# Optimization experiments

Hardware: AMD Instinct MI355X
Metric: run time of the kernel (lower is better)

The kernel has to match this reference:

```python
import jax, jax.numpy as jnp
import numpy as np

B, S, HIDDEN, NH = 2, 2048, 1024, 16
D = HIDDEN // NH  # 64
PHYS_W, CONS_W = 0.2, 0.15
LN_EPS = 1e-5


def _layernorm(x, gamma, beta):
    mu = jnp.mean(x, axis=-1, keepdims=True)
    var = jnp.mean(jnp.square(x - mu), axis=-1, keepdims=True)
    return (x - mu) * jax.lax.rsqrt(var + LN_EPS) * gamma + beta


def setup_inputs() -> dict:
    key = jax.random.key(0)
    ks = jax.random.split(key, 12)
    s = 0.02
    return {
        "cnn_features": jax.random.normal(ks[0], (B, S, HIDDEN), jnp.float32),
        "llm_features": jax.random.normal(ks[1], (B, S, HIDDEN), jnp.float32),
        # Linear weights stored [in, out] so y = x @ W + b (torch's W.T)
        "Wq": jax.random.normal(ks[2], (HIDDEN, HIDDEN), jnp.float32) * s,
        "bq": jnp.zeros((HIDDEN,), jnp.float32),
        "Wk": jax.random.normal(ks[3], (HIDDEN, HIDDEN), jnp.float32) * s,
        "bk": jnp.zeros((HIDDEN,), jnp.float32),
        "Wv": jax.random.normal(ks[4], (HIDDEN, HIDDEN), jnp.float32) * s,
        "bv": jnp.zeros((HIDDEN,), jnp.float32),
        "Wo": jax.random.normal(ks[5], (HIDDEN, HIDDEN), jnp.float32) * s,
        "bo": jnp.zeros((HIDDEN,), jnp.float32),
        "energy_emb": jax.random.normal(ks[6], (1, 1, HIDDEN), jnp.float32),
        "mass_emb": jax.random.normal(ks[7], (1, 1, HIDDEN), jnp.float32),
        "momentum_emb": jax.random.normal(ks[8], (1, 1, HIDDEN), jnp.float32),
        "gamma": jnp.ones((HIDDEN,), jnp.float32),
        "beta": jnp.zeros((HIDDEN,), jnp.float32),
    }


def reference(cnn_features, llm_features, Wq, bq, Wk, bk, Wv, bv, Wo, bo,
              energy_emb, mass_emb, momentum_emb, gamma, beta):
    Bsz, Sc, _ = cnn_features.shape
    Sl = llm_features.shape[1]

    def attn(q_in, kv_in):
        Sq, Sk = q_in.shape[1], kv_in.shape[1]
        Q = (q_in @ Wq + bq).reshape(Bsz, Sq, NH, D).transpose(0, 2, 1, 3)   # bhqd
        K = (kv_in @ Wk + bk).reshape(Bsz, Sk, NH, D).transpose(0, 2, 1, 3)  # bhkd
        V = (kv_in @ Wv + bv).reshape(Bsz, Sk, NH, D).transpose(0, 2, 1, 3)  # bhkd
        scores = jnp.einsum('bhqd,bhkd->bhqk', Q, K) / np.float32(np.sqrt(D))
        # physics biases: require Sq == Sk (elementwise Q*K), shape [B,H,Sq,1]
        energy_bias = jnp.sum(Q * K, axis=-1, keepdims=True) * PHYS_W
        mass_bias = jnp.mean(Q + K, axis=-1, keepdims=True) * CONS_W
        attn_w = jax.nn.softmax(scores + energy_bias + mass_bias, axis=-1)
        attended = jnp.einsum('bhqk,bhkd->bhqd', attn_w, V)
        attended = attended.transpose(0, 2, 1, 3).reshape(Bsz, Sq, HIDDEN)
        out = attended @ Wo + bo
        return _layernorm(q_in + out, gamma, beta)

    phys = jnp.concatenate([
        jnp.broadcast_to(energy_emb, (Bsz, 1, HIDDEN)),
        jnp.broadcast_to(mass_emb, (Bsz, 1, HIDDEN)),
        jnp.broadcast_to(momentum_emb, (Bsz, 1, HIDDEN)),
    ], axis=1)  # [B, 3, HIDDEN]
    aug_cnn = jnp.concatenate([cnn_features, phys], axis=1)  # [B, Sc+3, H]
    aug_llm = jnp.concatenate([llm_features, phys], axis=1)  # [B, Sl+3, H]

    cnn_att = attn(aug_cnn, aug_llm)
    llm_att = attn(aug_llm, aug_cnn)
    return cnn_att[:, :Sc, :], llm_att[:, :Sl, :]
```

## Files before the change

### kernel.cpp

```cpp
#include <hip/hip_runtime.h>

#define BN 2
#define SS 2048
#define SA 2051
#define HID 1024
#define NHD 16
#define DH 64
#define VTLD 8320
#define KSTR 72
#define VSTR 40
#define MFMA16 __builtin_amdgcn_mfma_f32_16x16x32_bf16
#define QSCALE 0.18033688011112042f

typedef __attribute__((ext_vector_type(4))) float floatx4;
typedef __attribute__((ext_vector_type(8))) short bf16x8;
typedef __attribute__((ext_vector_type(2))) unsigned uintx2;

__device__ __forceinline__ float bf2f(short s) {
  union { unsigned u; float f; } v; v.u = ((unsigned)(unsigned short)s) << 16; return v.f;
}
__device__ __forceinline__ short f2bf(float f) {
  union { float f; unsigned u; } v; v.f = f;
  unsigned u = v.u;
  u += 0x7FFF + ((u >> 16) & 1);
  return (short)(u >> 16);
}
__device__ __forceinline__ unsigned pack2(float lo, float hi) {
  unsigned ul = __float_as_uint(lo) + 0x8000u;
  unsigned uh = __float_as_uint(hi) + 0x8000u;
  return __builtin_amdgcn_perm(uh, ul, 0x07060302u);
}
__device__ __forceinline__ unsigned cvtpk(float lo, float hi) {
  unsigned r;
  asm("v_cvt_pk_bf16_f32 %0, %1, %2" : "=v"(r) : "v"(lo), "v"(hi));
  return r;
}
__device__ __forceinline__ float exp2fast(float x) {
#if __has_builtin(__builtin_amdgcn_exp2f)
  return __builtin_amdgcn_exp2f(x);
#else
  float r; asm("v_exp_f32 %0, %1" : "=v"(r) : "v"(x)); return r;
#endif
}
__device__ __forceinline__ uintx2 qtrans(unsigned A, unsigned B) {
  auto t = __builtin_amdgcn_permlane32_swap(A, B, false, false);
  auto u = __builtin_amdgcn_permlane16_swap(t[0], t[1], false, false);
  uintx2 r; r[0] = u[0]; r[1] = u[1];
  return r;
}
__device__ __forceinline__ void gload16(const short* g, short* l) {
  __builtin_amdgcn_global_load_lds(
      (const __attribute__((address_space(1))) void*)g,
      (__attribute__((address_space(3))) void*)l, 16, 0, 0);
}
__device__ __forceinline__ bool in_is_f32(const unsigned* graw) {
  return graw[0] == 0x3F800000u;
}

__global__ __launch_bounds__(256) void convert_in(const void* __restrict__ src, long off,
                                                  short* __restrict__ dst, int n,
                                                  const unsigned* __restrict__ graw) {
  bool f32 = in_is_f32(graw);
  int i = (blockIdx.x * 256 + threadIdx.x) * 4;
  int stride = gridDim.x * 1024;
  if (f32) {
    const float* s = (const float*)src + off;
    for (; i < n; i += stride) {
      float4 v = *(const float4*)(s + i);
      short4 o; o.x = f2bf(v.x); o.y = f2bf(v.y); o.z = f2bf(v.z); o.w = f2bf(v.w);
      *(short4*)(dst + i) = o;
    }
  } else {
    const short* s = (const short*)src + off;
    for (; i < n; i += stride)
      *(short4*)(dst + i) = *(const short4*)(s + i);
  }
}

__global__ __launch_bounds__(256) void convert_small(
    const void* s0, const void* s1, const void* s2, const void* s3,
    const void* s4, const void* s5, const void* s6, const void* s7,
    const void* s8, short* __restrict__ dst, const unsigned* __restrict__ graw) {
  bool f32 = in_is_f32(graw);
  const void* srcs[9] = {s0, s1, s2, s3, s4, s5, s6, s7, s8};
  const void* s = srcs[blockIdx.x];
  short* d = dst + (size_t)blockIdx.x * 1024;
  for (int i = threadIdx.x; i < 1024; i += 256)
    d[i] = f32 ? f2bf(((const float*)s)[i]) : ((const short*)s)[i];
}

__global__ __launch_bounds__(256) void conv_wt(const void* __restrict__ W,
    short* __restrict__ WT, const unsigned* __restrict__ graw) {
  __shared__ short tile[32][33];
  bool f32 = in_is_f32(graw);
  int n0 = blockIdx.x * 32, k0 = blockIdx.y * 32;
  int tx = threadIdx.x & 31, ty = threadIdx.x >> 5;
#pragma unroll
  for (int i = 0; i < 4; i++) {
    int k = k0 + ty + i*8;
    short v = f32 ? f2bf(((const float*)W)[(size_t)k * HID + n0 + tx])
                  : ((const short*)W)[(size_t)k * HID + n0 + tx];
    tile[ty + i*8][tx] = v;
  }
  __syncthreads();
#pragma unroll
  for (int i = 0; i < 4; i++)
    WT[(size_t)(n0 + ty + i*8) * HID + k0 + tx] = tile[tx][ty + i*8];
}

__device__ __forceinline__ void gemm_core_2ph(
    const short* apr0, const short* apr1,
    const short* bpr0, const short* bpr1,
    short* sA, short* sB, int wave, int l16, int quad, int msub, int nsub,
    floatx4 acc[4][4]) {
  gload16(apr0, sA + wave*512);  gload16(apr1, sA + 2048 + wave*512);
  gload16(bpr0, sB + wave*512);  gload16(bpr1, sB + 2048 + wave*512);
  int cur = 0;
  for (int k0 = 0; k0 < HID; k0 += 32) {
    if (k0 + 32 < HID) {
      int nx = cur ^ 1;
      gload16(apr0 + k0 + 32, sA + nx*4096 + wave*512);
      gload16(apr1 + k0 + 32, sA + nx*4096 + 2048 + wave*512);
      gload16(bpr0 + k0 + 32, sB + nx*4096 + wave*512);
      gload16(bpr1 + k0 + 32, sB + nx*4096 + 2048 + wave*512);
      asm volatile("s_waitcnt vmcnt(4)" ::: "memory");
    } else {
      asm volatile("s_waitcnt vmcnt(0)" ::: "memory");
    }
    __builtin_amdgcn_s_barrier();
    __builtin_amdgcn_sched_barrier(0);
    const short* cA = sA + cur*4096;
    const short* cB = sB + cur*4096;
    bf16x8 af[4], bf_[4];
#pragma unroll
    for (int i = 0; i < 4; i++) {
      af[i]  = *(const bf16x8*)(cA + (msub + i*16 + l16)*32 + quad*8);
      bf_[i] = *(const bf16x8*)(cB + (nsub + i*16 + l16)*32 + quad*8);
    }
#pragma unroll
    for (int mi = 0; mi < 4; mi++)
#pragma unroll
      for (int ni = 0; ni < 4; ni++)
        acc[mi][ni] = MFMA16(af[mi], bf_[ni], acc[mi][ni], 0, 0, 0);
    __builtin_amdgcn_sched_barrier(0);
    __builtin_amdgcn_s_barrier();
    __builtin_amdgcn_sched_barrier(0);
    cur ^= 1;
  }
}

__global__ __launch_bounds__(256) void gemm_qkv(
    const short* __restrict__ Xa, const short* __restrict__ WqT,
    const short* __restrict__ WkT, const short* __restrict__ WvT,
    const short* __restrict__ embB, const short* __restrict__ bqB,
    const short* __restrict__ bkB, const short* __restrict__ bvB,
    short* __restrict__ Qa, short* __restrict__ Ka, short* __restrict__ VT) {
  __shared__ __align__(16) short sA[2*4096];
  __shared__ __align__(16) short sB[2*4096];
  int t = threadIdx.x;
  int wave = t >> 6, lane = t & 63, l16 = lane & 15, quad = lane >> 4;
  int bid = blockIdx.x;
  int swz = (bid & 7) * 194 + (bid >> 3);

  const short *A, *B, *bias; short* out; long ldc;
  int m0, n0, tailA, tailB, bias_row; float scale;
  if (swz < 512) {
    A = Xa; B = WqT; bias = bqB; out = Qa; ldc = HID;
    m0 = (swz >> 3) * 128; n0 = (swz & 7) * 128;
    tailA = 0; tailB = 0; bias_row = 0; scale = QSCALE;
  } else if (swz < 1032) {
    int id = swz - 512;
    A = Xa; B = WkT; bias = bkB; out = Ka; ldc = HID;
    m0 = (id >> 3) * 128; n0 = (id & 7) * 128;
    tailA = 1; tailB = 0; bias_row = 0; scale = 1.f;
  } else {
    int id = swz - 1032;
    A = WvT; B = Xa; bias = bvB; out = VT; ldc = VTLD;
    m0 = (id / 65) * 128; n0 = (id % 65) * 128;
    tailA = 0; tailB = 1; bias_row = 1; scale = 1.f;
  }
  int msub = (wave >> 1) * 64, nsub = (wave & 1) * 64;

  const short* apr[2]; const short* bpr[2];
#pragma unroll
  for (int rep = 0; rep < 2; rep++) {
    int cid = rep * 256 + t;
    int row = cid >> 2, kc = (cid & 3) * 8;
    int ra = m0 + row;
    const short* ap;
    if (tailA && ra >= 8192) ap = embB + (size_t)((ra > 8194 ? 8194 : ra) - 8192) * 1024;
    else                     ap = A + (size_t)ra * HID;
    int rb = n0 + row;
    const short* bp;
    if (tailB && rb >= 8192) bp = embB + (size_t)((rb > 8194 ? 8194 : rb) - 8192) * 1024;
    else                     bp = B + (size_t)rb * HID;
    apr[rep] = ap + kc; bpr[rep] = bp + kc;
  }

  floatx4 acc[4][4] = {};
  gemm_core_2ph(apr[0], apr[1], bpr[0], bpr[1], sA, sB,
                wave, l16, quad, msub, nsub, acc);

#pragma unroll
  for (int mi = 0; mi < 4; mi++)
#pragma unroll
    for (int ni = 0; ni < 4; ni++) {
      int col = n0 + nsub + ni*16 + l16;
      float bcol = bias_row ? 0.f : bf2f(bias[col]);
#pragma unroll
      for (int r = 0; r < 4; r++) {
        int m = m0 + msub + mi*16 + quad*4 + r;
        float v = (acc[mi][ni][r] + (bias_row ? bf2f(bias[m]) : bcol)) * scale;
        out[(size_t)m * ldc + col] = f2bf(v);
      }
    }
}

__global__ __launch_bounds__(256) void gemm_bf(
    const short* __restrict__ A, const short* __restrict__ B,
    const short* __restrict__ bias, float scale,
    float* __restrict__ out32,
    const void* __restrict__ rc0, const void* __restrict__ rc1,
    const unsigned* __restrict__ graw) {
  __shared__ __align__(16) short sA[2*4096];
  __shared__ __align__(16) short sB[2*4096];
  int t = threadIdx.x;
  int wave = t >> 6, lane = t & 63, l16 = lane & 15, quad = lane >> 4;
  int nwg = gridDim.x * gridDim.y;
  int bid = blockIdx.y * gridDim.x + blockIdx.x;
  int cpx = nwg >> 3;
  int swz = (bid & 7) * cpx + (bid >> 3);
  int bx = swz % gridDim.x, by = swz / gridDim.x;
  int m0 = by * 128, n0 = bx * 128;
  int msub = (wave >> 1) * 64, nsub = (wave & 1) * 64;

  const short* apr[2]; const short* bpr[2];
#pragma unroll
  for (int rep = 0; rep < 2; rep++) {
    int cid = rep * 256 + t;
    int row = cid >> 2, kc = (cid & 3) * 8;
    apr[rep] = A + (size_t)(m0 + row) * HID + kc;
    bpr[rep] = B + (size_t)(n0 + row) * HID + kc;
  }

  floatx4 acc[4][4] = {};
  gemm_core_2ph(apr[0], apr[1], bpr[0], bpr[1], sA, sB,
                wave, l16, quad, msub, nsub, acc);

  bool f32in = in_is_f32(graw);
#pragma unroll
  for (int mi = 0; mi < 4; mi++)
#pragma unroll
    for (int ni = 0; ni < 4; ni++) {
      int col = n0 + nsub + ni*16 + l16;
      float bcol = bf2f(bias[col]);
#pragma unroll
      for (int r = 0; r < 4; r++) {
        int m = m0 + msub + mi*16 + quad*4 + r;
        float v = (acc[mi][ni][r] + bcol) * scale;
        float res;
        if (f32in) res = ((const float*)(m < 4096 ? rc0 : rc1))[(size_t)(m & 4095) * HID + col];
        else       res = bf2f(((const short*)(m < 4096 ? rc0 : rc1))[(size_t)(m & 4095) * HID + col]);
        out32[(size_t)m * HID + col] = v + res;
      }
    }
}

__global__ __launch_bounds__(256, 4) void flash3(
    const short* __restrict__ Qa, const short* __restrict__ Ka,
    const short* __restrict__ VTa, short* __restrict__ att) {
  __shared__ __align__(16) short sK0[32*KSTR], sK1[32*KSTR];
  __shared__ __align__(16) short sV0[64*VSTR], sV1[64*VSTR];
  int t = threadIdx.x, wave = t >> 6, lane = t & 63;
  int l16 = lane & 15, quad = lane >> 4;
  int bid = blockIdx.x;
  int swz = (bid & 7) * 128 + (bid >> 3);
  int qt  = swz & 15;
  int h   = (swz >> 4) & 15;
  int sb  = swz >> 8;
  int side = sb >> 1, b = sb & 1;
  int qrow0 = side * 4096 + b * 2048;
  int kvb = (side ^ 1) * 4096 + b * 2048;
  int q0 = qt * 128 + wave * 32;

  const short* qp0 = Qa + (size_t)(qrow0 + q0 + l16) * HID + h*DH + quad*8;
  const short* qp1 = qp0 + 16 * HID;
  bf16x8 qa0 = *(const bf16x8*)qp0, qb0 = *(const bf16x8*)(qp0 + 32);
  bf16x8 qa1 = *(const bf16x8*)qp1, qb1 = *(const bf16x8*)(qp1 + 32);

  float rs0 = 0.f, rs1 = 0.f;
  floatx4 oA[4] = {}, oB[4] = {};

  int krow = t >> 3, kc8 = (t & 7) * 8;
  int vrow = t >> 2, vc8 = (t & 3) * 8;
  const short* kgp = Ka + (size_t)(kvb + krow) * HID + h*DH + kc8;
  const short* vgp = VTa + (size_t)(h*DH + vrow) * VTLD + kvb + vc8;
  bf16x8 kreg = *(const bf16x8*)kgp;
  bf16x8 vreg = *(const bf16x8*)vgp;
  short *kw = sK0, *vw = sV0, *ka = sK1, *va = sV1;

  for (int kv0 = 0; kv0 < 2048; kv0 += 32) {
    *(bf16x8*)(kw + krow*KSTR + kc8) = kreg;
    *(bf16x8*)(vw + vrow*VSTR + vc8) = vreg;
    __syncthreads();
    kgp += 32*HID; vgp += 32;
    kreg = *(const bf16x8*)kgp;
    vreg = *(const bf16x8*)vgp;

    bf16x8 k00 = *(const bf16x8*)(kw + l16*KSTR + quad*8);
    bf16x8 k01 = *(const bf16x8*)(kw + l16*KSTR + 32 + quad*8);
    bf16x8 k10 = *(const bf16x8*)(kw + (16 + l16)*KSTR + quad*8);
    bf16x8 k11 = *(const bf16x8*)(kw + (16 + l16)*KSTR + 32 + quad*8);
    bf16x8 v0 = *(const bf16x8*)(vw + l16*VSTR + quad*8);
    bf16x8 v1 = *(const bf16x8*)(vw + (16 + l16)*VSTR + quad*8);
    bf16x8 v2 = *(const bf16x8*)(vw + (32 + l16)*VSTR + quad*8);
    bf16x8 v3 = *(const bf16x8*)(vw + (48 + l16)*VSTR + quad*8);

    floatx4 s00 = {}, s10 = {}, s01 = {}, s11 = {};
    __builtin_amdgcn_s_setprio(1);
    s00 = MFMA16(k00, qa0, s00, 0, 0, 0); s00 = MFMA16(k01, qb0, s00, 0, 0, 0);
    s10 = MFMA16(k10, qa0, s10, 0, 0, 0); s10 = MFMA16(k11, qb0, s10, 0, 0, 0);
    s01 = MFMA16(k00, qa1, s01, 0, 0, 0); s01 = MFMA16(k01, qb1, s01, 0, 0, 0);
    s11 = MFMA16(k10, qa1, s11, 0, 0, 0); s11 = MFMA16(k11, qb1, s11, 0, 0, 0);
    __builtin_amdgcn_s_setprio(0);

    floatx4 p00, p10, p01, p11;
#pragma unroll
    for (int r = 0; r < 4; r++) {
      p00[r] = exp2fast(s00[r]); p10[r] = exp2fast(s10[r]);
      p01[r] = exp2fast(s01[r]); p11[r] = exp2fast(s11[r]);
    }
    rs0 += ((p00[0]+p00[1])+(p00[2]+p00[3])) + ((p10[0]+p10[1])+(p10[2]+p10[3]));
    rs1 += ((p01[0]+p01[1])+(p01[2]+p01[3])) + ((p11[0]+p11[1])+(p11[2]+p11[3]));

    unsigned pc00 = cvtpk(p00[0], p00[1]), pc01 = cvtpk(p00[2], p00[3]);
    unsigned pc10 = cvtpk(p10[0], p10[1]), pc11 = cvtpk(p10[2], p10[3]);
    unsigned pd00 = cvtpk(p01[0], p01[1]), pd01 = cvtpk(p01[2], p01[3]);
    unsigned pd10 = cvtpk(p11[0], p11[1]), pd11 = cvtpk(p11[2], p11[3]);
    uintx2 uA0 = qtrans(pc00, pc10);
    uintx2 uA1 = qtrans(pc01, pc11);
    uintx2 uB0 = qtrans(pd00, pd10);
    uintx2 uB1 = qtrans(pd01, pd11);
    union { unsigned u[4]; bf16x8 v; } pf0, pf1;
    pf0.u[0] = uA0[0]; pf0.u[1] = uA1[0]; pf0.u[2] = uA0[1]; pf0.u[3] = uA1[1];
    pf1.u[0] = uB0[0]; pf1.u[1] = uB1[0]; pf1.u[2] = uB0[1]; pf1.u[3] = uB1[1];

    __builtin_amdgcn_s_setprio(1);
    oA[0] = MFMA16(v0, pf0.v, oA[0], 0, 0, 0);
    oA[1] = MFMA16(v1, pf0.v, oA[1], 0, 0, 0);
    oA[2] = MFMA16(v2, pf0.v, oA[2], 0, 0, 0);
    oA[3] = MFMA16(v3, pf0.v, oA[3], 0, 0, 0);
    oB[0] = MFMA16(v0, pf1.v, oB[0], 0, 0, 0);
    oB[1] = MFMA16(v1, pf1.v, oB[1], 0, 0, 0);
    oB[2] = MFMA16(v2, pf1.v, oB[2], 0, 0, 0);
    oB[3] = MFMA16(v3, pf1.v, oB[3], 0, 0, 0);
    __builtin_amdgcn_s_setprio(0);

    short* tk = kw; kw = ka; ka = tk;
    short* tv = vw; vw = va; va = tv;
  }

  {
    int er = l16 < 2 ? l16 : 2;
    const short* kpt = Ka + (size_t)(8192 + er) * HID + h*DH + quad*8;
    bf16x8 tk0 = *(const bf16x8*)kpt;
    bf16x8 tk1 = *(const bf16x8*)(kpt + 32);
    floatx4 s00 = {}, s01 = {};
    s00 = MFMA16(tk0, qa0, s00, 0, 0, 0); s00 = MFMA16(tk1, qb0, s00, 0, 0, 0);
    s01 = MFMA16(tk0, qa1, s01, 0, 0, 0); s01 = MFMA16(tk1, qb1, s01, 0, 0, 0);
    floatx4 p00, p01;
#pragma unroll
    for (int r = 0; r < 4; r++) {
      bool val = (quad == 0) && (r < 3);
      p00[r] = val ? exp2fast(s00[r]) : 0.f;
      p01[r] = val ? exp2fast(s01[r]) : 0.f;
    }
    rs0 += (p00[0]+p00[1]) + (p00[2]+p00[3]);
    rs1 += (p01[0]+p01[1]) + (p01[2]+p01[3]);
    unsigned pc00 = cvtpk(p00[0], p00[1]), pc01 = cvtpk(p00[2], p00[3]);
    unsigned pd00 = cvtpk(p01[0], p01[1]), pd01 = cvtpk(p01[2], p01[3]);
    uintx2 uA0 = qtrans(pc00, 0u);
    uintx2 uA1 = qtrans(pc01, 0u);
    uintx2 uB0 = qtrans(pd00, 0u);
    uintx2 uB1 = qtrans(pd01, 0u);
    union { unsigned u[4]; bf16x8 v; } pf0, pf1;
    pf0.u[0] = uA0[0]; pf0.u[1] = uA1[0]; pf0.u[2] = uA0[1]; pf0.u[3] = uA1[1];
    pf1.u[0] = uB0[0]; pf1.u[1] = uB1[0]; pf1.u[2] = uB0[1]; pf1.u[3] = uB1[1];
    const short* vtp = VTa + (size_t)(h*DH + l16) * VTLD + 8192 + quad*8;
    bf16x8 v0 = *(const bf16x8*)vtp;
    bf16x8 v1 = *(const bf16x8*)(vtp + 16*VTLD);
    bf16x8 v2 = *(const bf16x8*)(vtp + 32*VTLD);
    bf16x8 v3 = *(const bf16x8*)(vtp + 48*VTLD);
    oA[0] = MFMA16(v0, pf0.v, oA[0], 0, 0, 0);
    oA[1] = MFMA16(v1, pf0.v, oA[1], 0, 0, 0);
    oA[2] = MFMA16(v2, pf0.v, oA[2], 0, 0, 0);
    oA[3] = MFMA16(v3, pf0.v, oA[3], 0, 0, 0);
    oB[0] = MFMA16(v0, pf1.v, oB[0], 0, 0, 0);
    oB[1] = MFMA16(v1, pf1.v, oB[1], 0, 0, 0);
    oB[2] = MFMA16(v2, pf1.v, oB[2], 0, 0, 0);
    oB[3] = MFMA16(v3, pf1.v, oB[3], 0, 0, 0);
  }

  rs0 += __shfl_xor(rs0, 16, 64); rs0 += __shfl_xor(rs0, 32, 64);
  rs1 += __shfl_xor(rs1, 16, 64); rs1 += __shfl_xor(rs1, 32, 64);
  float i0 = 1.f / rs0, i1 = 1.f / rs1;

  unsigned* ob0 = (unsigned*)(att + (size_t)(qrow0 + q0 + l16) * HID + h*DH + quad*4);
  unsigned* ob1 = (unsigned*)(att + (size_t)(qrow0 + q0 + 16 + l16) * HID + h*DH + quad*4);
#pragma unroll
  for (int n = 0; n < 4; n++) {
    ob0[n*8]     = pack2(oA[n][0]*i0, oA[n][1]*i0);
    ob0[n*8 + 1] = pack2(oA[n][2]*i0, oA[n][3]*i0);
    ob1[n*8]     = pack2(oB[n][0]*i1, oB[n][1]*i1);
    ob1[n*8 + 1] = pack2(oB[n][2]*i1, oB[n][3]*i1);
  }
}

__global__ __launch_bounds__(256) void ln_kernel(
    const float* __restrict__ y, const short* __restrict__ gamma,
    const short* __restrict__ beta, void* __restrict__ outp, long orow,
    const unsigned* __restrict__ graw) {
  bool f32o = in_is_f32(graw);
  int row = blockIdx.x;
  int t = threadIdx.x;
  const float* yr = y + (size_t)row * HID;
  float4 v = ((const float4*)yr)[t];
  float sum = v.x + v.y + v.z + v.w;
#pragma unroll
  for (int off = 32; off >= 1; off >>= 1) sum += __shfl_xor(sum, off, 64);
  __shared__ float red[8];
  int wave = t >> 6, lane = t & 63;
  if (lane == 0) red[wave] = sum;
  __syncthreads();
  float mu = (red[0] + red[1] + red[2] + red[3]) * (1.f/HID);
  float dx = v.x - mu, dy = v.y - mu, dz = v.z - mu, dw = v.w - mu;
  float sq = dx*dx + dy*dy + dz*dz + dw*dw;
#pragma unroll
  for (int off = 32; off >= 1; off >>= 1) sq += __shfl_xor(sq, off, 64);
  if (lane == 0) red[4 + wave] = sq;
  __syncthreads();
  float var = (red[4] + red[5] + red[6] + red[7]) * (1.f/HID);
  float inv = rsqrtf(var + 1e-5f);
  const short* g = gamma + t*4;
  const short* be = beta + t*4;
  float o0 = dx * inv * bf2f(g[0]) + bf2f(be[0]);
  float o1 = dy * inv * bf2f(g[1]) + bf2f(be[1]);
  float o2 = dz * inv * bf2f(g[2]) + bf2f(be[2]);
  float o3 = dw * inv * bf2f(g[3]) + bf2f(be[3]);
  size_t base = (size_t)(orow + row) * HID + t*4;
  if (f32o) {
    float4 ov = {o0, o1, o2, o3};
    *(float4*)((float*)outp + base) = ov;
  } else {
    short4 ov = {f2bf(o0), f2bf(o1), f2bf(o2), f2bf(o3)};
    *(short4*)((short*)outp + base) = ov;
  }
}

extern "C" void kernel_launch(void* const* d_in, const int* in_sizes, int n_in,
                              void* d_out, int out_size, void* d_ws, size_t ws_size,
                              hipStream_t stream) {
  const void* cnn = d_in[0];
  const void* llm = d_in[1];
  const void* Wq  = d_in[2];
  const void* bq  = d_in[3];
  const void* Wk  = d_in[4];
  const void* bk  = d_in[5];
  const void* Wv  = d_in[6];
  const void* bv  = d_in[7];
  const void* Wo  = d_in[8];
  const void* bo  = d_in[9];
  const void* ee  = d_in[10];
  const void* me  = d_in[11];
  const void* pe  = d_in[12];
  const void* gamma = d_in[13];
  const void* beta  = d_in[14];
  const unsigned* graw = (const unsigned*)gamma;
  (void)in_sizes; (void)n_in; (void)out_size; (void)ws_size;

  char* p = (char*)d_ws;
  auto alloc = [&](size_t bytes) { char* r = p; p += (bytes + 255) & ~(size_t)255; return r; };
  short* WqT = (short*)alloc((size_t)HID*HID*2);
  short* WkT = (short*)alloc((size_t)HID*HID*2);
  short* WvT = (short*)alloc((size_t)HID*HID*2);
  short* WoT = (short*)alloc((size_t)HID*HID*2);
  short* smallB = (short*)alloc(9 * 1024 * 2);
  short* Qa  = (short*)alloc((size_t)8192 * HID * 2);
  short* Ka  = (short*)alloc((size_t)8320 * HID * 2);
  short* VT  = (short*)alloc((size_t)HID * VTLD * 2);
  float* y   = (float*)Qa;
  short* att = (short*)d_out;
  short* Xa  = (short*)d_out + (size_t)8192 * HID;
  short* bqB = smallB;        short* bkB = smallB + 1024;
  short* bvB = smallB + 2048; short* boB = smallB + 3072;
  short* embB = smallB + 4096;
  short* gB  = smallB + 7168; short* bB  = smallB + 8192;

  dim3 tb(256);
  dim3 tg(32, 32);
  const int NF = 4096 * HID;

  convert_in<<<dim3(NF/1024), tb, 0, stream>>>(cnn, 0, Xa, NF, graw);
  convert_in<<<dim3(NF/1024), tb, 0, stream>>>(llm, 0, Xa + (size_t)NF, NF, graw);
  conv_wt<<<tg, tb, 0, stream>>>(Wq, WqT, graw);
  conv_wt<<<tg, tb, 0, stream>>>(Wk, WkT, graw);
  conv_wt<<<tg, tb, 0, stream>>>(Wv, WvT, graw);
  conv_wt<<<tg, tb, 0, stream>>>(Wo, WoT, graw);
  convert_small<<<dim3(9), tb, 0, stream>>>(bq, bk, bv, bo, ee, me, pe, gamma, beta,
                                            smallB, graw);

  gemm_qkv<<<dim3(1552), tb, 0, stream>>>(Xa, WqT, WkT, WvT, embB,
                                          bqB, bkB, bvB, Qa, Ka, VT);

  flash3<<<dim3(1024), tb, 0, stream>>>(Qa, Ka, VT, att);

  gemm_bf<<<dim3(8, 64), tb, 0, stream>>>(att, WoT, boB, 1.f, y, cnn, llm, graw);

  ln_kernel<<<dim3(8192), tb, 0, stream>>>(y, gB, bB, d_out, 0, graw);
}
```

Before: 371.4 us.

## Merge conversion launches and swizzle GEMM LDS tile layout to avoid bank conflicts

Result: faster. 353.6 us (-4.8%).

```diff
diff --git a/kernel.cpp b/kernel.cpp
--- a/kernel.cpp
+++ b/kernel.cpp
@@ -57,23 +57,20 @@
   return graw[0] == 0x3F800000u;
 }
 
-__global__ __launch_bounds__(256) void convert_in(const void* __restrict__ src, long off,
-                                                  short* __restrict__ dst, int n,
-                                                  const unsigned* __restrict__ graw) {
+__global__ __launch_bounds__(256) void convert_in2(
+    const void* __restrict__ s0, const void* __restrict__ s1,
+    short* __restrict__ dst, const unsigned* __restrict__ graw) {
   bool f32 = in_is_f32(graw);
+  const int NF = 4096 * HID;
   int i = (blockIdx.x * 256 + threadIdx.x) * 4;
-  int stride = gridDim.x * 1024;
+  const void* s = i < NF ? s0 : s1;
+  int j = i < NF ? i : i - NF;
   if (f32) {
-    const float* s = (const float*)src + off;
-    for (; i < n; i += stride) {
-      float4 v = *(const float4*)(s + i);
-      short4 o; o.x = f2bf(v.x); o.y = f2bf(v.y); o.z = f2bf(v.z); o.w = f2bf(v.w);
-      *(short4*)(dst + i) = o;
-    }
+    float4 v = *(const float4*)((const float*)s + j);
+    short4 o; o.x = f2bf(v.x); o.y = f2bf(v.y); o.z = f2bf(v.z); o.w = f2bf(v.w);
+    *(short4*)(dst + i) = o;
   } else {
-    const short* s = (const short*)src + off;
-    for (; i < n; i += stride)
-      *(short4*)(dst + i) = *(const short4*)(s + i);
+    *(short4*)(dst + i) = *(const short4*)((const short*)s + j);
   }
 }
 
@@ -89,10 +86,15 @@
     d[i] = f32 ? f2bf(((const float*)s)[i]) : ((const short*)s)[i];
 }
 
-__global__ __launch_bounds__(256) void conv_wt(const void* __restrict__ W,
+__global__ __launch_bounds__(256) void conv_wt4(
+    const void* __restrict__ W0, const void* __restrict__ W1,
+    const void* __restrict__ W2, const void* __restrict__ W3,
     short* __restrict__ WT, const unsigned* __restrict__ graw) {
   __shared__ short tile[32][33];
   bool f32 = in_is_f32(graw);
+  const void* Ws[4] = {W0, W1, W2, W3};
+  const void* W = Ws[blockIdx.z];
+  short* dst = WT + (size_t)blockIdx.z * HID * HID;
   int n0 = blockIdx.x * 32, k0 = blockIdx.y * 32;
   int tx = threadIdx.x & 31, ty = threadIdx.x >> 5;
 #pragma unroll
@@ -105,7 +107,7 @@
   __syncthreads();
 #pragma unroll
   for (int i = 0; i < 4; i++)
-    WT[(size_t)(n0 + ty + i*8) * HID + k0 + tx] = tile[tx][ty + i*8];
+    dst[(size_t)(n0 + ty + i*8) * HID + k0 + tx] = tile[tx][ty + i*8];
 }
 
 __device__ __forceinline__ void gemm_core_2ph(
@@ -115,6 +117,7 @@
     floatx4 acc[4][4]) {
   gload16(apr0, sA + wave*512);  gload16(apr1, sA + 2048 + wave*512);
   gload16(bpr0, sB + wave*512);  gload16(bpr1, sB + 2048 + wave*512);
+  int p8 = ((quad + (l16 >> 1)) & 3) * 8;
   int cur = 0;
   for (int k0 = 0; k0 < HID; k0 += 32) {
     if (k0 + 32 < HID) {
@@ -134,8 +137,8 @@
     bf16x8 af[4], bf_[4];
 #pragma unroll
     for (int i = 0; i < 4; i++) {
-      af[i]  = *(const bf16x8*)(cA + (msub + i*16 + l16)*32 + quad*8);
-      bf_[i] = *(const bf16x8*)(cB + (nsub + i*16 + l16)*32 + quad*8);
+      af[i]  = *(const bf16x8*)(cA + (msub + i*16 + l16)*32 + p8);
+      bf_[i] = *(const bf16x8*)(cB + (nsub + i*16 + l16)*32 + p8);
     }
 #pragma unroll
     for (int mi = 0; mi < 4; mi++)
@@ -181,11 +184,12 @@
   }
   int msub = (wave >> 1) * 64, nsub = (wave & 1) * 64;
 
+  int kc = (((lane & 3) - ((lane >> 3) & 3)) & 3) * 8;
   const short* apr[2]; const short* bpr[2];
 #pragma unroll
   for (int rep = 0; rep < 2; rep++) {
     int cid = rep * 256 + t;
-    int row = cid >> 2, kc = (cid & 3) * 8;
+    int row = cid >> 2;
     int ra = m0 + row;
     const short* ap;
     if (tailA && ra >= 8192) ap = embB + (size_t)((ra > 8194 ? 8194 : ra) - 8192) * 1024;
@@ -234,11 +238,12 @@
   int m0 = by * 128, n0 = bx * 128;
   int msub = (wave >> 1) * 64, nsub = (wave & 1) * 64;
 
+  int kc = (((lane & 3) - ((lane >> 3) & 3)) & 3) * 8;
   const short* apr[2]; const short* bpr[2];
 #pragma unroll
   for (int rep = 0; rep < 2; rep++) {
     int cid = rep * 256 + t;
-    int row = cid >> 2, kc = (cid & 3) * 8;
+    int row = cid >> 2;
     apr[rep] = A + (size_t)(m0 + row) * HID + kc;
     bpr[rep] = B + (size_t)(n0 + row) * HID + kc;
   }
@@ -497,15 +502,10 @@
   short* gB  = smallB + 7168; short* bB  = smallB + 8192;
 
   dim3 tb(256);
-  dim3 tg(32, 32);
   const int NF = 4096 * HID;
 
-  convert_in<<<dim3(NF/1024), tb, 0, stream>>>(cnn, 0, Xa, NF, graw);
-  convert_in<<<dim3(NF/1024), tb, 0, stream>>>(llm, 0, Xa + (size_t)NF, NF, graw);
-  conv_wt<<<tg, tb, 0, stream>>>(Wq, WqT, graw);
-  conv_wt<<<tg, tb, 0, stream>>>(Wk, WkT, graw);
-  conv_wt<<<tg, tb, 0, stream>>>(Wv, WvT, graw);
-  conv_wt<<<tg, tb, 0, stream>>>(Wo, WoT, graw);
+  convert_in2<<<dim3(2*NF/1024), tb, 0, stream>>>(cnn, llm, Xa, graw);
+  conv_wt4<<<dim3(32, 32, 4), tb, 0, stream>>>(Wq, Wk, Wv, Wo, WqT, graw);
   convert_small<<<dim3(9), tb, 0, stream>>>(bq, bk, bv, bo, ee, me, pe, gamma, beta,
                                             smallB, graw);
 
```
